# Optimization experiments

Hardware: AMD Instinct MI355X
Metric: run time of the kernel (lower is better)

## Reference

```python
import jax, jax.numpy as jnp
import numpy as np

B = 16384
IN = 1024
H = 1024
LN_EPS = 1e-5


def setup_inputs() -> dict:
    key = jax.random.key(0)
    ks = jax.random.split(key, 8)
    # Five gate Linears fused into one weight [IN+H, 5H] (order: f, i, o, c, m)
    scale = 1.0 / np.sqrt(IN + H)
    W = jax.random.uniform(ks[0], (IN + H, 5 * H), jnp.float32, -scale, scale)
    b = jax.random.uniform(ks[1], (5 * H,), jnp.float32, -scale, scale)
    return {
        "x": jax.random.normal(ks[2], (B, IN), jnp.float32),
        "h_prev": jax.random.normal(ks[3], (B, H), jnp.float32),
        "c_prev": jax.random.normal(ks[4], (B, H), jnp.float32),
        "W": W,
        "b": b,
        "ln_gamma": jnp.ones((H,), jnp.float32),
        "ln_beta": jnp.zeros((H,), jnp.float32),
        "retention": jnp.full((H,), 0.9, jnp.float32),
    }


def _layernorm(z, gamma, beta):
    mu = jnp.mean(z, axis=-1, keepdims=True)
    var = jnp.var(z, axis=-1, keepdims=True)
    return (z - mu) * jax.lax.rsqrt(var + LN_EPS) * gamma + beta


def reference(x, h_prev, c_prev, W, b, ln_gamma, ln_beta, retention):
    combined = jnp.concatenate([x, h_prev], axis=-1)        # [B, IN+H]
    gates = combined @ W + b                                # [B, 5H] fused GEMM
    f_pre, i_pre, o_pre, c_pre_act, m_pre = jnp.split(gates, 5, axis=-1)
    f_gate = jax.nn.sigmoid(f_pre)
    i_gate = jax.nn.sigmoid(i_pre)
    o_gate = jax.nn.sigmoid(o_pre)
    c_cand = jnp.tanh(c_pre_act)
    m_gate = jax.nn.sigmoid(m_pre)
    c_new = f_gate * c_prev + i_gate * c_cand
    c_new = c_new * retention + (1.0 - retention) * c_prev
    c_new = m_gate * c_new + (1.0 - m_gate) * c_prev
    # exp(ln)/(1+exp(ln)) == sigmoid(layernorm(o_gate))
    o_exp = jax.nn.sigmoid(_layernorm(o_gate, ln_gamma, ln_beta))
    h_new = o_exp * jnp.tanh(c_new)
    return h_new, c_new
```

## Files before the change

kernel.cpp:

```cpp
#include <hip/hip_runtime.h>
#include <math.h>


typedef unsigned short u16;
typedef unsigned int   u32;
typedef short  short8 __attribute__((ext_vector_type(8)));
typedef float  f32x4  __attribute__((ext_vector_type(4)));
typedef u16    u16x4  __attribute__((ext_vector_type(4)));
typedef u32    u32x4  __attribute__((ext_vector_type(4)));

#define B_ROWS 16384
#define K_DIM  2048
#define N_DIM  5120
#define H_DIM  1024

__device__ __forceinline__ float b2f(u16 u) {
    u32 v = ((u32)u) << 16;
    return __uint_as_float(v);
}
__device__ __forceinline__ u16 f2b(float f) {
    u32 x = __float_as_uint(f);
    u32 r = (x + 0x7fffu + ((x >> 16) & 1u)) >> 16;
    return (u16)r;
}
__device__ __forceinline__ float sigm(float v) {
    return 1.f / (1.f + __expf(-v));
}
__device__ __forceinline__ float tanh_fast(float v) {
    v = fminf(fmaxf(v, -15.f), 15.f);
    float e = __expf(-2.f * v);
    return (1.f - e) / (1.f + e);
}

__global__ __launch_bounds__(256) void convert_A(const float* __restrict__ x,
                                                 const float* __restrict__ h,
                                                 u16* __restrict__ A) {
    size_t idx = ((size_t)blockIdx.x * 256 + threadIdx.x) * 8;
    int row = (int)(idx >> 11);
    int col = (int)(idx & 2047);
    const float* src = (col < 1024) ? (x + (size_t)row * 1024 + col)
                                    : (h + (size_t)row * 1024 + (col - 1024));
    f32x4 v0 = *(const f32x4*)src;
    f32x4 v1 = *(const f32x4*)(src + 4);
    u32x4 w;
    w.x = (u32)f2b(v0.x) | ((u32)f2b(v0.y) << 16);
    w.y = (u32)f2b(v0.z) | ((u32)f2b(v0.w) << 16);
    w.z = (u32)f2b(v1.x) | ((u32)f2b(v1.y) << 16);
    w.w = (u32)f2b(v1.z) | ((u32)f2b(v1.w) << 16);
    *(u32x4*)(A + idx) = w;
}

__global__ __launch_bounds__(256) void convert_W(const float* __restrict__ W,
                                                 u16* __restrict__ Wt) {
    __shared__ float tile[32][33];
    int tx = threadIdx.x & 31;
    int ty = threadIdx.x >> 5;
    int n0 = blockIdx.x * 32;
    int k0 = blockIdx.y * 32;
#pragma unroll
    for (int i = 0; i < 4; ++i)
        tile[ty + 8 * i][tx] = W[(size_t)(k0 + ty + 8 * i) * N_DIM + n0 + tx];
    __syncthreads();
#pragma unroll
    for (int i = 0; i < 4; ++i)
        Wt[(size_t)(n0 + ty + 8 * i) * K_DIM + k0 + tx] = f2b(tile[tx][ty + 8 * i]);
}

#define BK 32
#define NBUF 4

__device__ __forceinline__ void gld_lds16(const void* g, void* l) {
    __builtin_amdgcn_global_load_lds(
        (const __attribute__((address_space(1))) void*)g,
        (__attribute__((address_space(3))) void*)l, 16, 0, 0);
}

__global__ __launch_bounds__(512, 2) void gemm_gates(const u16* __restrict__ A,
                                                     const u16* __restrict__ Bt,
                                                     const float* __restrict__ bias,
                                                     u16* __restrict__ gates) {
    __shared__ u16 lds[NBUF][2][256 * BK];

    const int t = threadIdx.x;
    const int bid = blockIdx.x;
    const int swz = (bid & 7) * 160 + (bid >> 3);
    const int m0 = (swz & 63) << 8;
    const int n0 = (swz >> 6) << 8;

    const int l   = t & 63;
    const int wid = t >> 6;
    const int wm  = (wid >> 2) << 7;
    const int wn  = (wid & 3) << 6;
    const int lr  = l & 15;
    const int lh  = l >> 4;

    f32x4 acc[8][4] = {};

    const int sRow = t >> 2;
    const int sCol = (t & 3) * 8;
    const u16* aBase = A  + (size_t)(m0 + sRow) * K_DIM + sCol;
    const u16* bBase = Bt + (size_t)(n0 + sRow) * K_DIM + sCol;
    const int ldsOff = t * 8;

#define STAGE(kt, buf)                                                        \
    do {                                                                      \
        const u16* a_ = aBase + (kt) * BK;                                    \
        const u16* b_ = bBase + (kt) * BK;                                    \
        gld_lds16(a_,                        &lds[buf][0][ldsOff]);           \
        gld_lds16(a_ + (size_t)128 * K_DIM,  &lds[buf][0][ldsOff + 4096]);    \
        gld_lds16(b_,                        &lds[buf][1][ldsOff]);           \
        gld_lds16(b_ + (size_t)128 * K_DIM,  &lds[buf][1][ldsOff + 4096]);    \
    } while (0)

    STAGE(0, 0);
    STAGE(1, 1);
    STAGE(2, 2);
    __builtin_amdgcn_sched_barrier(0);
    asm volatile("s_waitcnt vmcnt(8)" ::: "memory");
    __builtin_amdgcn_s_barrier();
    __builtin_amdgcn_sched_barrier(0);

    const int NKT = K_DIM / BK;
    for (int kt = 0; kt < NKT; ++kt) {
        const int buf = kt & (NBUF - 1);
        if (kt + 3 < NKT) STAGE(kt + 3, (kt + 3) & (NBUF - 1));

        const u16* As = lds[buf][0];
        const u16* Bs = lds[buf][1];
        short8 af[8], bf[4];
#pragma unroll
        for (int ni = 0; ni < 4; ++ni)
            bf[ni] = *(const short8*)&Bs[(wn + ni * 16 + lr) * BK + lh * 8];
#pragma unroll
        for (int mi = 0; mi < 8; ++mi)
            af[mi] = *(const short8*)&As[(wm + mi * 16 + lr) * BK + lh * 8];

        __builtin_amdgcn_s_setprio(1);
#pragma unroll
        for (int mi = 0; mi < 8; ++mi)
#pragma unroll
            for (int ni = 0; ni < 4; ++ni)
                acc[mi][ni] = __builtin_amdgcn_mfma_f32_16x16x32_bf16(
                    af[mi], bf[ni], acc[mi][ni], 0, 0, 0);
        __builtin_amdgcn_s_setprio(0);

        __builtin_amdgcn_sched_barrier(0);
        if (kt < NKT - 3) {
            asm volatile("s_waitcnt vmcnt(8)" ::: "memory");
        } else {
            asm volatile("s_waitcnt vmcnt(0)" ::: "memory");
        }
        __builtin_amdgcn_s_barrier();
        __builtin_amdgcn_sched_barrier(0);
    }
#undef STAGE

    const int grp = n0 >> 10;
#pragma unroll
    for (int ni = 0; ni < 4; ++ni) {
        int col = n0 + wn + ni * 16 + lr;
        float bv = bias[col];
#pragma unroll
        for (int mi = 0; mi < 8; ++mi) {
#pragma unroll
            for (int j = 0; j < 4; ++j) {
                int row = m0 + wm + mi * 16 + lh * 4 + j;
                float v = acc[mi][ni][j] + bv;
                float g = (grp == 3) ? tanh_fast(v) : sigm(v);
                gates[(size_t)row * N_DIM + col] = f2b(g);
            }
        }
    }
}

__global__ __launch_bounds__(256) void fuse_out(const u16* __restrict__ gates,
                                                const float* __restrict__ c_prev,
                                                const float* __restrict__ ret,
                                                const float* __restrict__ gamma,
                                                const float* __restrict__ beta,
                                                float* __restrict__ out) {
    const int r = blockIdx.x;
    const int t = threadIdx.x;
    const u16* g = gates + (size_t)r * N_DIM;
    const int j0 = t * 4;

    u16x4 ov = *(const u16x4*)(g + 2048 + j0);
    float o0 = b2f(ov.x), o1 = b2f(ov.y), o2 = b2f(ov.z), o3 = b2f(ov.w);
    float s1 = o0 + o1 + o2 + o3;
    float s2 = o0 * o0 + o1 * o1 + o2 * o2 + o3 * o3;
#pragma unroll
    for (int off = 32; off; off >>= 1) {
        s1 += __shfl_xor(s1, off, 64);
        s2 += __shfl_xor(s2, off, 64);
    }
    __shared__ float red[8];
    if ((t & 63) == 0) { red[t >> 6] = s1; red[4 + (t >> 6)] = s2; }
    __syncthreads();
    float S1 = red[0] + red[1] + red[2] + red[3];
    float S2 = red[4] + red[5] + red[6] + red[7];
    float mu   = S1 * (1.f / 1024.f);
    float var  = S2 * (1.f / 1024.f) - mu * mu;
    float rstd = rsqrtf(var + 1e-5f);

    u16x4 fv = *(const u16x4*)(g + j0);
    u16x4 iv = *(const u16x4*)(g + 1024 + j0);
    u16x4 cv = *(const u16x4*)(g + 3072 + j0);
    u16x4 mv = *(const u16x4*)(g + 4096 + j0);
    f32x4 cp = *(const f32x4*)(c_prev + (size_t)r * H_DIM + j0);
    f32x4 rt = *(const f32x4*)(ret + j0);
    f32x4 gm = *(const f32x4*)(gamma + j0);
    f32x4 bt = *(const f32x4*)(beta + j0);

    float of[4] = {o0, o1, o2, o3};
    u16 fa[4] = {fv.x, fv.y, fv.z, fv.w};
    u16 ia[4] = {iv.x, iv.y, iv.z, iv.w};
    u16 ca[4] = {cv.x, cv.y, cv.z, cv.w};
    u16 ma[4] = {mv.x, mv.y, mv.z, mv.w};

    f32x4 hout, cout;
#pragma unroll
    for (int i = 0; i < 4; ++i) {
        float f = b2f(fa[i]), ig = b2f(ia[i]), cc = b2f(ca[i]), m = b2f(ma[i]);
        float cpv = cp[i], rv = rt[i];
        float c1 = f * cpv + ig * cc;
        float c2 = c1 * rv + (1.f - rv) * cpv;
        float cn = m * c2 + (1.f - m) * cpv;
        float ln = (of[i] - mu) * rstd * gm[i] + bt[i];
        float oe = sigm(ln);
        float hn = oe * tanh_fast(cn);
        hout[i] = hn;
        cout[i] = cn;
    }
    *(f32x4*)(out + (size_t)r * H_DIM + j0) = hout;
    *(f32x4*)(out + (size_t)B_ROWS * H_DIM + (size_t)r * H_DIM + j0) = cout;
}

extern "C" void kernel_launch(void* const* d_in, const int* in_sizes, int n_in,
                              void* d_out, int out_size, void* d_ws, size_t ws_size,
                              hipStream_t stream) {
    const float* x      = (const float*)d_in[0];
    const float* h_prev = (const float*)d_in[1];
    const float* c_prev = (const float*)d_in[2];
    const float* W      = (const float*)d_in[3];
    const float* bias   = (const float*)d_in[4];
    const float* gamma  = (const float*)d_in[5];
    const float* beta   = (const float*)d_in[6];
    const float* ret    = (const float*)d_in[7];
    float* out = (float*)d_out;

    u16* Abuf  = (u16*)d_ws;
    u16* Wt    = Abuf + (size_t)B_ROWS * K_DIM;
    u16* gates = Wt + (size_t)N_DIM * K_DIM;

    convert_A<<<(B_ROWS * K_DIM / 8) / 256, 256, 0, stream>>>(x, h_prev, Abuf);
    convert_W<<<dim3(N_DIM / 32, K_DIM / 32), 256, 0, stream>>>(W, Wt);
    gemm_gates<<<(B_ROWS / 256) * (N_DIM / 256), 512, 0, stream>>>(Abuf, Wt, bias, gates);
    fuse_out<<<B_ROWS, 256, 0, stream>>>(gates, c_prev, ret, gamma, beta, out);
}
```

Measured before the change: 517.9 us.

## Pre-swizzle A and W layouts globally, use BK=64 double-buffered GEMM pipeline

The conversion kernels now write A and the transposed W with an XOR swizzle of 8-element chunks within each 64-wide K block. This lets the GEMM copy straight into LDS with global_load_lds and read fragments without bank conflicts. The GEMM moves from a 4-stage BK=32 pipeline to a 2-stage BK=64 double buffer and splits the A fragment loads into two halves to reduce register pressure. convert_W also writes 16-byte vectors. The trade-off is a shallower prefetch depth and an extra barrier per K step.

```diff
diff --git a/kernel.cpp b/kernel.cpp
--- a/kernel.cpp
+++ b/kernel.cpp
@@ -38,8 +38,9 @@
     size_t idx = ((size_t)blockIdx.x * 256 + threadIdx.x) * 8;
     int row = (int)(idx >> 11);
     int col = (int)(idx & 2047);
-    const float* src = (col < 1024) ? (x + (size_t)row * 1024 + col)
-                                    : (h + (size_t)row * 1024 + (col - 1024));
+    int srcCol = (col & ~63) | (((((col >> 3) & 7) ^ (row & 7))) << 3);
+    const float* src = (srcCol < 1024) ? (x + (size_t)row * 1024 + srcCol)
+                                       : (h + (size_t)row * 1024 + (srcCol - 1024));
     f32x4 v0 = *(const f32x4*)src;
     f32x4 v1 = *(const f32x4*)(src + 4);
     u32x4 w;
@@ -52,22 +53,28 @@
 
 __global__ __launch_bounds__(256) void convert_W(const float* __restrict__ W,
                                                  u16* __restrict__ Wt) {
-    __shared__ float tile[32][33];
-    int tx = threadIdx.x & 31;
-    int ty = threadIdx.x >> 5;
-    int n0 = blockIdx.x * 32;
-    int k0 = blockIdx.y * 32;
-#pragma unroll
-    for (int i = 0; i < 4; ++i)
+    __shared__ float tile[64][33];
+    const int t  = threadIdx.x;
+    const int tx = t & 31;
+    const int ty = t >> 5;
+    const int n0 = blockIdx.x * 32;
+    const int k0 = blockIdx.y * 64;
+#pragma unroll
+    for (int i = 0; i < 8; ++i)
         tile[ty + 8 * i][tx] = W[(size_t)(k0 + ty + 8 * i) * N_DIM + n0 + tx];
     __syncthreads();
-#pragma unroll
-    for (int i = 0; i < 4; ++i)
-        Wt[(size_t)(n0 + ty + 8 * i) * K_DIM + k0 + tx] = f2b(tile[tx][ty + 8 * i]);
-}
-
-#define BK 32
-#define NBUF 4
+    const int n = t >> 3;
+    const int s = t & 7;
+    const int g = s ^ (n & 7);
+    u32x4 w;
+    w.x = (u32)f2b(tile[g * 8 + 0][n]) | ((u32)f2b(tile[g * 8 + 1][n]) << 16);
+    w.y = (u32)f2b(tile[g * 8 + 2][n]) | ((u32)f2b(tile[g * 8 + 3][n]) << 16);
+    w.z = (u32)f2b(tile[g * 8 + 4][n]) | ((u32)f2b(tile[g * 8 + 5][n]) << 16);
+    w.w = (u32)f2b(tile[g * 8 + 6][n]) | ((u32)f2b(tile[g * 8 + 7][n]) << 16);
+    *(u32x4*)(Wt + (size_t)(n0 + n) * K_DIM + k0 + s * 8) = w;
+}
+
+#define BK 64
 
 __device__ __forceinline__ void gld_lds16(const void* g, void* l) {
     __builtin_amdgcn_global_load_lds(
@@ -79,7 +86,7 @@
                                                      const u16* __restrict__ Bt,
                                                      const float* __restrict__ bias,
                                                      u16* __restrict__ gates) {
-    __shared__ u16 lds[NBUF][2][256 * BK];
+    __shared__ u16 lds[2][2][256 * BK];
 
     const int t = threadIdx.x;
     const int bid = blockIdx.x;
@@ -89,85 +96,97 @@
 
     const int l   = t & 63;
     const int wid = t >> 6;
-    const int wm  = (wid >> 2) << 7;
-    const int wn  = (wid & 3) << 6;
+    const int wr  = wid >> 2;
+    const int wc  = wid & 3;
     const int lr  = l & 15;
     const int lh  = l >> 4;
+    const int z   = lr & 7;
+    const int sA0 = (lh ^ z) * 8;
+
+    const int sRow = t >> 3;
+    const int sOff = (t & 7) * 8;
+    const u16* aBase = A  + (size_t)(m0 + sRow) * K_DIM + sOff;
+    const u16* bBase = Bt + (size_t)(n0 + sRow) * K_DIM + sOff;
+    const int dOff = t * 8;
 
     f32x4 acc[8][4] = {};
 
-    const int sRow = t >> 2;
-    const int sCol = (t & 3) * 8;
-    const u16* aBase = A  + (size_t)(m0 + sRow) * K_DIM + sCol;
-    const u16* bBase = Bt + (size_t)(n0 + sRow) * K_DIM + sCol;
-    const int ldsOff = t * 8;
-
-#define STAGE(kt, buf)                                                        \
-    do {                                                                      \
-        const u16* a_ = aBase + (kt) * BK;                                    \
-        const u16* b_ = bBase + (kt) * BK;                                    \
-        gld_lds16(a_,                        &lds[buf][0][ldsOff]);           \
-        gld_lds16(a_ + (size_t)128 * K_DIM,  &lds[buf][0][ldsOff + 4096]);    \
-        gld_lds16(b_,                        &lds[buf][1][ldsOff]);           \
-        gld_lds16(b_ + (size_t)128 * K_DIM,  &lds[buf][1][ldsOff + 4096]);    \
-    } while (0)
+#define STAGE(kt, buf) do {                                                   \
+    _Pragma("unroll") for (int i = 0; i < 4; ++i) {                           \
+        gld_lds16(aBase + (size_t)(i * 64) * K_DIM + (kt) * BK,               \
+                  &lds[buf][0][dOff + i * 4096]);                             \
+        gld_lds16(bBase + (size_t)(i * 64) * K_DIM + (kt) * BK,               \
+                  &lds[buf][1][dOff + i * 4096]);                             \
+    }                                                                         \
+} while (0)
 
     STAGE(0, 0);
-    STAGE(1, 1);
-    STAGE(2, 2);
-    __builtin_amdgcn_sched_barrier(0);
-    asm volatile("s_waitcnt vmcnt(8)" ::: "memory");
-    __builtin_amdgcn_s_barrier();
-    __builtin_amdgcn_sched_barrier(0);
-
-    const int NKT = K_DIM / BK;
-    for (int kt = 0; kt < NKT; ++kt) {
-        const int buf = kt & (NBUF - 1);
-        if (kt + 3 < NKT) STAGE(kt + 3, (kt + 3) & (NBUF - 1));
-
-        const u16* As = lds[buf][0];
-        const u16* Bs = lds[buf][1];
-        short8 af[8], bf[4];
-#pragma unroll
-        for (int ni = 0; ni < 4; ++ni)
-            bf[ni] = *(const short8*)&Bs[(wn + ni * 16 + lr) * BK + lh * 8];
-#pragma unroll
-        for (int mi = 0; mi < 8; ++mi)
-            af[mi] = *(const short8*)&As[(wm + mi * 16 + lr) * BK + lh * 8];
-
-        __builtin_amdgcn_s_setprio(1);
-#pragma unroll
-        for (int mi = 0; mi < 8; ++mi)
-#pragma unroll
-            for (int ni = 0; ni < 4; ++ni)
-                acc[mi][ni] = __builtin_amdgcn_mfma_f32_16x16x32_bf16(
-                    af[mi], bf[ni], acc[mi][ni], 0, 0, 0);
-        __builtin_amdgcn_s_setprio(0);
-
-        __builtin_amdgcn_sched_barrier(0);
-        if (kt < NKT - 3) {
+
+#pragma unroll 1
+    for (int kt = 0; kt < 32; ++kt) {
+        const int cur = kt & 1;
+        if (kt < 31) {
+            STAGE(kt + 1, cur ^ 1);
+            __builtin_amdgcn_sched_barrier(0);
             asm volatile("s_waitcnt vmcnt(8)" ::: "memory");
         } else {
+            __builtin_amdgcn_sched_barrier(0);
             asm volatile("s_waitcnt vmcnt(0)" ::: "memory");
         }
-        __builtin_amdgcn_s_barrier();
+        asm volatile("s_barrier" ::: "memory");
         __builtin_amdgcn_sched_barrier(0);
+
+        const u16* As = lds[cur][0];
+        const u16* Bs = lds[cur][1];
+        short8 bf[4][2], af[4][2];
+#pragma unroll
+        for (int ni = 0; ni < 4; ++ni) {
+            const int u = (wc * 64 + ni * 16 + lr) * BK;
+            bf[ni][0] = *(const short8*)&Bs[u + sA0];
+            bf[ni][1] = *(const short8*)&Bs[u + (sA0 ^ 32)];
+        }
+#pragma unroll
+        for (int q = 0; q < 2; ++q) {
+#pragma unroll
+            for (int m = 0; m < 4; ++m) {
+                const int u = (wr * 128 + q * 64 + m * 16 + lr) * BK;
+                af[m][0] = *(const short8*)&As[u + sA0];
+                af[m][1] = *(const short8*)&As[u + (sA0 ^ 32)];
+            }
+            __builtin_amdgcn_s_setprio(1);
+#pragma unroll
+            for (int sk = 0; sk < 2; ++sk)
+#pragma unroll
+                for (int m = 0; m < 4; ++m)
+#pragma unroll
+                    for (int ni = 0; ni < 4; ++ni)
+                        acc[q * 4 + m][ni] = __builtin_amdgcn_mfma_f32_16x16x32_bf16(
+                            af[m][sk], bf[ni][sk], acc[q * 4 + m][ni], 0, 0, 0);
+            __builtin_amdgcn_s_setprio(0);
+        }
+
+        __builtin_amdgcn_sched_barrier(0);
+        asm volatile("s_barrier" ::: "memory");
+        __builtin_amdgcn_sched_barrier(0);
     }
 #undef STAGE
 
     const int grp = n0 >> 10;
 #pragma unroll
     for (int ni = 0; ni < 4; ++ni) {
-        int col = n0 + wn + ni * 16 + lr;
+        int col = n0 + wc * 64 + ni * 16 + lr;
         float bv = bias[col];
 #pragma unroll
-        for (int mi = 0; mi < 8; ++mi) {
-#pragma unroll
-            for (int j = 0; j < 4; ++j) {
-                int row = m0 + wm + mi * 16 + lh * 4 + j;
-                float v = acc[mi][ni][j] + bv;
-                float g = (grp == 3) ? tanh_fast(v) : sigm(v);
-                gates[(size_t)row * N_DIM + col] = f2b(g);
+        for (int q = 0; q < 2; ++q) {
+#pragma unroll
+            for (int m = 0; m < 4; ++m) {
+#pragma unroll
+                for (int j = 0; j < 4; ++j) {
+                    int row = m0 + wr * 128 + q * 64 + m * 16 + lh * 4 + j;
+                    float v = acc[q * 4 + m][ni][j] + bv;
+                    float g = (grp == 3) ? tanh_fast(v) : sigm(v);
+                    gates[(size_t)row * N_DIM + col] = f2b(g);
+                }
             }
         }
     }
@@ -253,7 +272,7 @@
     u16* gates = Wt + (size_t)N_DIM * K_DIM;
 
     convert_A<<<(B_ROWS * K_DIM / 8) / 256, 256, 0, stream>>>(x, h_prev, Abuf);
-    convert_W<<<dim3(N_DIM / 32, K_DIM / 32), 256, 0, stream>>>(W, Wt);
+    convert_W<<<dim3(N_DIM / 32, K_DIM / 64), 256, 0, stream>>>(W, Wt);
     gemm_gates<<<(B_ROWS / 256) * (N_DIM / 256), 512, 0, stream>>>(Abuf, Wt, bias, gates);
     fuse_out<<<B_ROWS, 256, 0, stream>>>(gates, c_prev, ret, gamma, beta, out);
 }
```

Measured after the change: 499.8 us. -3.5%, faster.
